# Performance work log

Measured on AMD Instinct MI355X. Metric: run time of the kernel, lower is better.

Reference implementation:

```python
import jax, jax.numpy as jnp
import numpy as np


def _cd2(a, b):
    # squared euclidean distances [n,m]
    d = jnp.sum(a * a, 1)[:, None] + jnp.sum(b * b, 1)[None, :] - 2.0 * (a @ b.T)
    return jnp.maximum(d, 0.0)


def _cdist(a, b):
    # tiny clamp keeps sqrt grad finite on the zero diagonal, fwd unchanged
    return jnp.sqrt(jnp.maximum(_cd2(a, b), 1e-30))


def _tmedian(x):
    # torch.median semantics: lower middle element
    f = jnp.sort(x.reshape(-1))
    return f[(f.shape[0] - 1) // 2]


def setup_inputs() -> dict:
    key = jax.random.key(0)
    k1, k2 = jax.random.split(key)
    feat_s = jax.random.normal(k1, (25, 640), dtype=jnp.float32)
    y_s = (jnp.arange(25) % 5).astype(jnp.int32)  # 5-way 5-shot, every class present
    feat_q = jax.random.normal(k2, (300, 640), dtype=jnp.float32)
    return {"feat_s": feat_s, "y_s": y_s, "feat_q": feat_q}


def reference(feat_s, y_s, feat_q):
    y_s_np = np.asarray(y_s)
    classes = np.unique(y_s_np)
    C = int(classes.shape[0])
    onehot = jnp.asarray(y_s_np[:, None] == classes[None, :], dtype=feat_s.dtype)  # [S,C]
    prototypes = (onehot.T @ feat_s) / jnp.sum(onehot, 0)[:, None]  # [C,D]

    # ---- virtual mixup densification ----
    dist_q = _cdist(feat_q, prototypes)  # [Nq,C]
    y_boot = np.asarray(jnp.argmin(dist_q, 1))
    q_norm = feat_q / jnp.linalg.norm(feat_q, axis=1, keepdims=True)
    cos_np = np.asarray(q_norm @ q_norm.T)
    dist_q_np = np.asarray(dist_q)
    virt = []
    for c in range(C):
        idx = np.flatnonzero(y_boot == c)
        if idx.size < 2:
            continue
        cos_c = cos_np[np.ix_(idx, idx)]
        f = np.sort(cos_c.reshape(-1))
        thresh = f[(f.size - 1) // 2]  # torch lower median
        ii, jj = np.nonzero(np.triu(cos_c >= thresh, 1))  # pairs with i<j
        if ii.size:
            virt.append(0.5 * (feat_q[idx[ii]] + feat_q[idx[jj]]))
        kq = int(idx[np.argmin(dist_q_np[idx, c])])
        virt.append((0.5 * (prototypes[c] + feat_q[kq]))[None, :])
    feat_all = jnp.concatenate([feat_q] + virt, 0) if virt else feat_q

    # ---- self-tuning affinity (kNN graph) ----
    n = int(feat_all.shape[0])
    k = max(1, int(np.log2(n)))
    dist = _cdist(feat_all, feat_all)  # [n,n]
    _, nn_idx = jax.lax.top_k(-dist, k + 1)  # smallest k+1 (incl. self)
    sigma = dist[jnp.arange(n), nn_idx[:, k]] + 1e-8
    nbrs = nn_idx[:, 1:]  # [n,k]
    d_nb = jnp.take_along_axis(dist, nbrs, 1)
    w = jnp.exp(-d_nb / (sigma[:, None] * sigma[nbrs]))
    W = jnp.zeros((n, n), feat_all.dtype).at[jnp.arange(n)[:, None], nbrs].set(w)
    W = (W + W.T) / 2
    D_inv = 1.0 / (W.sum(1) + 1e-8)

    # ---- density-adaptive lambda ----
    d = _cdist(feat_all, prototypes).min(1)
    lam = jnp.exp(-(d ** 2) / (2 * _tmedian(d) ** 2 + 1e-8))

    # ---- mm iterations (label propagation) ----
    a = _cd2(feat_all, prototypes)  # [n,C]
    y0 = jax.nn.softmax(-a, axis=1)
    scale = (lam * D_inv)[:, None]

    def step(carry, _):
        y, done = carry
        y_new = jax.nn.softmax(-a + scale * (W @ y), axis=1)
        conv = jnp.max(jnp.abs(y_new - y)) < 1e-4
        y_out = jnp.where(done | conv, y, y_new)  # emulate torch early break
        return (y_out, done | conv), None

    (y, _), _ = jax.lax.scan(step, (y0, jnp.asarray(False)), None, length=50)
    preds = jnp.argmax(y[: feat_q.shape[0]], 1)
    return preds
```

## Files before the change

### kernel.cpp

```cpp
#include <hip/hip_runtime.h>
#include <math.h>

#define CMAX 8
#define KMAX 16
#define TPB 256
#define BNMAX 1024

struct P {
  const float* fs; const int* ys; const float* fq;
  int S, Q, D, BN, NMAX;
  float* proto;
  float* G;
  float* cosq;
  int* cls; int* scount; int* qcount; int* qidx; int* kq;
  float* thr;
  int* rowcnt; int* rowoff; int* paircnt; int* basev;
  int* meta;
  int* uv;
  float* rn2;
  int* cand;
  int* nbrs; float* dnb; float* wgt; float* sigma;
  int* indeg; int* inoff; int* cursor;
  int* insrcU; float* inwU; int* indst;
  int2* inedge;
  unsigned* cosk;
  unsigned* gmaxu;
  float* amat; float* dinv; float* dmin; float* scalev;
  float* yA; float* yB;
  float* meddenom;
  int* outp;
};

__device__ inline unsigned f2key(float f){
  unsigned b=__float_as_uint(f);
  return (b&0x80000000u)? ~b : (b|0x80000000u);
}
__device__ inline float key2f(unsigned k){
  unsigned b=(k&0x80000000u)? (k^0x80000000u) : ~k;
  return __uint_as_float(b);
}
__device__ inline unsigned long long shfl_xor_u64(unsigned long long v,int m){
  unsigned lo=(unsigned)v, hi=(unsigned)(v>>32);
  lo=__shfl_xor(lo,m,64); hi=__shfl_xor(hi,m,64);
  return (((unsigned long long)hi)<<32)|lo;
}

__global__ void k_init(P p){
  if (threadIdx.x==0){
    int labs[CMAX]; int cnt[CMAX]; int C=0;
    for (int s=0;s<p.S;s++){
      int l=p.ys[s]; int f=-1;
      for(int c=0;c<C;c++) if(labs[c]==l){f=c;break;}
      if(f<0){ if(C<CMAX){labs[C]=l;cnt[C]=1;C++;} }
      else cnt[f]++;
    }
    for(int a=0;a<C;a++)for(int b=a+1;b<C;b++)
      if(labs[b]<labs[a]){int t=labs[a];labs[a]=labs[b];labs[b]=t;
                          t=cnt[a];cnt[a]=cnt[b];cnt[b]=t;}
    for(int c=0;c<C;c++){p.cls[c]=labs[c];p.scount[c]=cnt[c];}
    p.meta[0]=C;
  }
}

__global__ void k_proto(P p){
  int c=blockIdx.x; int C=p.meta[0];
  for(int d=threadIdx.x; d<p.D; d+=blockDim.x){
    float s=0.f;
    if(c<C){
      int lab=p.cls[c];
      for(int j=0;j<p.S;j++) if(p.ys[j]==lab) s+=p.fs[(size_t)j*p.D+d];
      s/= (float)p.scount[c];
    }
    p.proto[(size_t)c*p.D+d]=s;
  }
}

__global__ void k_gram(P p){
  __shared__ float arow[1024];
  int a=blockIdx.x;
  const float* ra = (a<p.Q)? p.fq + (size_t)a*p.D : p.proto + (size_t)(a-p.Q)*p.D;
  const float* A = ra;
  if(p.D<=1024){
    for(int d=threadIdx.x; d<p.D; d+=blockDim.x) arow[d]=ra[d];
    __syncthreads();
    A=(const float*)arow;
  }
  int D4=p.D>>2; int Dt=D4<<2;
  for(int b=threadIdx.x; b<p.BN; b+=blockDim.x){
    const float* rb=(b<p.Q)? p.fq+(size_t)b*p.D : p.proto+(size_t)(b-p.Q)*p.D;
    const float4* a4=(const float4*)A;
    const float4* b4=(const float4*)rb;
    float s=0.f;
    #pragma unroll 4
    for(int d=0;d<D4;d++){
      float4 x=a4[d], y=b4[d];
      s += x.x*y.x + x.y*y.y + x.z*y.z + x.w*y.w;
    }
    for(int d=Dt;d<p.D;d++) s += A[d]*rb[d];
    p.G[(size_t)a*p.BN+b]=s;
  }
}

__global__ void k_cos(P p){
  int t=blockIdx.x*blockDim.x+threadIdx.x;
  if(t>=p.Q*p.Q)return;
  int i=t/p.Q, j=t%p.Q;
  p.cosq[t]=p.G[(size_t)i*p.BN+j]/(sqrtf(p.G[(size_t)i*p.BN+i])*sqrtf(p.G[(size_t)j*p.BN+j]));
}

__global__ void k_qidx(P p){
  int c=blockIdx.x; int C=p.meta[0];
  int lane=threadIdx.x;
  if(c>=C){ if(lane==0){p.qcount[c]=0;p.kq[c]=0;} return; }
  int base=0;
  for(int q0=0;q0<p.Q;q0+=64){
    int q=q0+lane;
    bool in=false;
    if(q<p.Q){
      float gq=p.G[(size_t)q*p.BN+q];
      float best=INFINITY; int bc=0;
      for(int cc=0;cc<C;cc++){
        int pc=p.Q+cc;
        float d2=fmaxf(gq+p.G[(size_t)pc*p.BN+pc]-2.f*p.G[(size_t)q*p.BN+pc],0.f);
        if(d2<best){best=d2;bc=cc;}
      }
      in=(bc==c);
    }
    unsigned long long mask=__ballot(in);
    int pre=__popcll(mask & ((lane==63)?0x7FFFFFFFFFFFFFFFull:((1ull<<lane)-1ull)));
    if(in) p.qidx[c*p.Q+base+pre]=q;
    base+=__popcll(mask);
  }
  if(lane==0) p.qcount[c]=base;
  int pc=p.Q+c;
  float gp=p.G[(size_t)pc*p.BN+pc];
  unsigned long long best=0xFFFFFFFFFFFFFFFFull;
  for(int t=lane;t<base;t+=64){
    int q=p.qidx[c*p.Q+t];
    float d2=fmaxf(p.G[(size_t)q*p.BN+q]+gp-2.f*p.G[(size_t)q*p.BN+pc],0.f);
    unsigned long long key=(((unsigned long long)f2key(d2))<<32)|(unsigned)t;
    if(key<best)best=key;
  }
  #pragma unroll
  for(int s=32;s>=1;s>>=1){
    unsigned long long o=shfl_xor_u64(best,s);
    if(o<best)best=o;
  }
  if(lane==0){
    int t=(int)(unsigned)(best&0xFFFFFFFFull);
    p.kq[c]=(base>0)? p.qidx[c*p.Q+t] : 0;
  }
}

__global__ void k_median(P p){
  __shared__ unsigned hist[256];
  __shared__ unsigned sPref; __shared__ int sTrem;
  __shared__ int sqidx[512];
  int c=blockIdx.x; int C=p.meta[0];
  int m=(c<C)? p.qcount[c]:0;
  int tid=threadIdx.x;
  if(m<2){ if(tid==0) p.thr[c]=INFINITY; return; }
  const int* qix;
  if(p.Q<=512){
    for(int t=tid;t<m;t+=blockDim.x) sqidx[t]=p.qidx[c*p.Q+t];
    __syncthreads();
    qix=sqidx;
  } else qix=p.qidx+c*p.Q;
  int total=m*m;
  unsigned* keys=p.cosk+(size_t)c*p.Q*p.Q;
  for(int t=tid;t<total;t+=blockDim.x){
    int a=t/m, b=t-a*m;
    keys[t]=f2key(p.cosq[(size_t)qix[a]*p.Q+qix[b]]);
  }
  if(tid==0){ sPref=0u; sTrem=(total-1)/2; }
  __syncthreads();
  unsigned prefmask=0u;
  for(int shift=24;shift>=0;shift-=8){
    hist[tid&255]=0u;
    __syncthreads();
    unsigned pref=sPref;
    for(int t=tid;t<total;t+=blockDim.x){
      unsigned key=keys[t];
      if((key&prefmask)==pref) atomicAdd(&hist[(key>>shift)&255],1u);
    }
    __syncthreads();
    if(tid==0){
      int trem=sTrem; unsigned cum=0;
      for(int b=0;b<256;b++){
        unsigned h=hist[b];
        if(cum+h>(unsigned)trem){ sPref=pref|((unsigned)b<<shift); sTrem=trem-(int)cum; break; }
        cum+=h;
      }
    }
    __syncthreads();
    prefmask|=(0xFFu<<shift);
  }
  if(tid==0) p.thr[c]=key2f(sPref);
}

__global__ void k_rowcnt(P p){
  int c=blockIdx.x; int C=p.meta[0];
  int m=(c<C)? p.qcount[c]:0;
  if(m<2){ if(threadIdx.x==0) p.paircnt[c]=0; return; }
  float th=p.thr[c];
  for(int a=threadIdx.x;a<m;a+=blockDim.x){
    int ia=p.qidx[c*p.Q+a]; int cnt=0;
    const float* row=p.cosq+(size_t)ia*p.Q;
    for(int b=a+1;b<m;b++){
      int ib=p.qidx[c*p.Q+b];
      cnt += (row[ib]>=th);
    }
    p.rowcnt[c*p.Q+a]=cnt;
  }
  __syncthreads();
  if(threadIdx.x==0){
    int run=0;
    for(int a=0;a<m;a++){p.rowoff[c*p.Q+a]=run; run+=p.rowcnt[c*p.Q+a];}
    p.paircnt[c]=run;
  }
}

__global__ void k_bases(P p){
  int C=p.meta[0]; int cur=p.Q;
  for(int c=0;c<C;c++){
    p.basev[c]=cur;
    if(p.qcount[c]>=2) cur += p.paircnt[c]+1;
  }
  int n=cur; if(n>p.NMAX)n=p.NMAX;
  p.meta[1]=n;
  int k=31-__clz(n); if(k<1)k=1; if(k>KMAX-1)k=KMAX-1;
  p.meta[2]=k;
  p.meta[3]=0;
  p.meta[4]=0;
  p.meta[5]=0;
  for(int t=0;t<64;t++) p.gmaxu[t]=0u;
}

__global__ void k_uv(P p){
  int r=blockIdx.x*blockDim.x+threadIdx.x;
  if(r>=p.NMAX)return;
  p.indeg[r]=0;
  if(r<p.Q){ p.uv[2*r]=r; p.uv[2*r+1]=r; }
}

__global__ void k_uvpairs(P p){
  int c=blockIdx.x; int C=p.meta[0];
  int m=(c<C)? p.qcount[c]:0;
  if(m<2)return;
  float th=p.thr[c];
  int bs=p.basev[c];
  for(int a=threadIdx.x;a<m;a+=blockDim.x){
    int ia=p.qidx[c*p.Q+a];
    int off=bs+p.rowoff[c*p.Q+a]; int cnt=0;
    const float* row=p.cosq+(size_t)ia*p.Q;
    for(int b=a+1;b<m;b++){
      int ib=p.qidx[c*p.Q+b];
      if(row[ib]>=th){
        int r=off+cnt;
        p.uv[2*r]=ia; p.uv[2*r+1]=ib;
        cnt++;
      }
    }
  }
  if(threadIdx.x==0){
    int r=bs+p.paircnt[c];
    p.uv[2*r]=p.Q+c; p.uv[2*r+1]=p.kq[c];
  }
}

__global__ void k_rn2c(P p){
  int r=blockIdx.x*blockDim.x+threadIdx.x;
  int n=p.meta[1]; if(r>=n)return;
  int u=p.uv[2*r],v=p.uv[2*r+1];
  float hu=0.5f*(p.G[(size_t)u*p.BN+u]+p.G[(size_t)v*p.BN+u]);
  float hv=0.5f*(p.G[(size_t)u*p.BN+v]+p.G[(size_t)v*p.BN+v]);
  float rn=0.5f*(hu+hv);
  p.rn2[r]=rn;
  ((int4*)p.cand)[r]=make_int4(u,v,__float_as_int(rn),0);
}

template<int KSEL>
__device__ void knn_scan(const P& p,int n,int kp1,const float* sh,bool useSh,
                         const float* Gu,const float* Gv,float rni,
                         unsigned long long* wl){
  int lane=threadIdx.x&63; int w=threadIdx.x>>6;
  unsigned kf[KSEL]; int kj[KSEL];
  #pragma unroll
  for(int t=0;t<KSEL;t++){ kf[t]=0xFFFFFFFFu; kj[t]=0x7FFFFFFF; }
  unsigned thrw=0xFFFFFFFFu;
  int iters=(n+127)>>7;
  const int4* cand=(const int4*)p.cand;
  for(int it=0;it<iters;++it){
    int j=(it<<7)+(w<<6)+lane;
    unsigned key=0xFFFFFFFFu;
    if(j<n){
      int4 cd=cand[j];
      float dot = useSh ? (sh[cd.x]+sh[cd.y])
                        : 0.5f*(Gu[cd.x]+Gv[cd.x])+0.5f*(Gu[cd.y]+Gv[cd.y]);
      float d2=fmaxf(rni+__int_as_float(cd.z)-dot,0.f);
      key=__float_as_uint(d2);
    }
    if(key<=thrw && key<kf[KSEL-1]){
      int cj=j;
      #pragma unroll
      for(int t=0;t<KSEL;t++){
        bool lt = key<kf[t];
        unsigned nk = lt? key : kf[t];
        unsigned ok = lt? kf[t] : key;
        int nj = lt? cj : kj[t];
        int oj = lt? kj[t] : cj;
        kf[t]=nk; kj[t]=nj; key=ok; cj=oj;
      }
    }
    if((it&7)==7){
      unsigned v=kf[KSEL-1];
      #pragma unroll
      for(int s=32;s>=1;s>>=1){
        unsigned o=(unsigned)__shfl_xor((int)v,s,64);
        if(o<v)v=o;
      }
      thrw=v;
    }
  }
  for(int t=0;t<kp1;t++){
    unsigned long long mv=(((unsigned long long)kf[0])<<32)|(unsigned)kj[0];
    unsigned long long m=mv;
    #pragma unroll
    for(int s=32;s>=1;s>>=1){
      unsigned long long o=shfl_xor_u64(m,s);
      if(o<m)m=o;
    }
    if(mv==m){
      #pragma unroll
      for(int q=0;q<KSEL-1;q++){ kf[q]=kf[q+1]; kj[q]=kj[q+1]; }
      kf[KSEL-1]=0xFFFFFFFFu; kj[KSEL-1]=0x7FFFFFFF;
    }
    if(lane==0) wl[w*16+t]=m;
  }
}

__global__ void __launch_bounds__(128) k_knn(P p){
  __shared__ float sh[BNMAX];
  __shared__ unsigned long long wl[32];
  int i=blockIdx.x;
  int n=p.meta[1]; if(i>=n)return;
  int kp1=p.meta[2]+1;
  int u1=p.uv[2*i], v1=p.uv[2*i+1];
  const float* Gu=p.G+(size_t)u1*p.BN;
  const float* Gv=p.G+(size_t)v1*p.BN;
  bool useSh=(p.BN<=BNMAX);
  if(useSh){
    for(int d=threadIdx.x; d<p.BN; d+=128) sh[d]=0.5f*(Gu[d]+Gv[d]);
  }
  __syncthreads();
  float rni=p.rn2[i];
  if(kp1<=13) knn_scan<13>(p,n,kp1,sh,useSh,Gu,Gv,rni,wl);
  else        knn_scan<16>(p,n,kp1,sh,useSh,Gu,Gv,rni,wl);
  __syncthreads();
  if(threadIdx.x==0){
    int a=0,b=0;
    for(int t=0;t<kp1;t++){
      unsigned long long va=wl[a], vb=wl[16+b];
      unsigned long long m;
      if(va<=vb){m=va;a++;} else {m=vb;b++;}
      int j=(int)(unsigned)(m&0xFFFFFFFFull);
      float d2=__uint_as_float((unsigned)(m>>32));
      float dd=sqrtf(fmaxf(d2,1e-30f));
      if(t>=1){ p.nbrs[(size_t)i*KMAX+t-1]=j; p.dnb[(size_t)i*KMAX+t-1]=dd; }
      if(t==kp1-1) p.sigma[i]=dd+1e-8f;
    }
  }
}

__global__ void k_wgtcnt(P p){
  int i=blockIdx.x*blockDim.x+threadIdx.x;
  int n=p.meta[1]; if(i>=n)return;
  int k=p.meta[2];
  float si=p.sigma[i];
  for(int q=0;q<k;q++){
    int j=p.nbrs[(size_t)i*KMAX+q];
    p.wgt[(size_t)i*KMAX+q]=expf(-p.dnb[(size_t)i*KMAX+q]/(si*p.sigma[j]));
    atomicAdd(&p.indeg[j],1);
  }
  for(int q=k;q<KMAX;q++){ p.nbrs[(size_t)i*KMAX+q]=i; p.wgt[(size_t)i*KMAX+q]=0.f; }
}

__global__ void k_scan(P p){
  __shared__ int part[TPB];
  int n=p.meta[1];
  int chunk=(n+TPB-1)/TPB;
  int beg=threadIdx.x*chunk, end=beg+chunk; if(end>n)end=n;
  int s=0;
  for(int i=beg;i<end;i++) s+=p.indeg[i];
  part[threadIdx.x]=s; __syncthreads();
  if(threadIdx.x==0){
    int run=0;
    for(int t=0;t<TPB;t++){int v=part[t];part[t]=run;run+=v;}
    p.inoff[n]=run;
  }
  __syncthreads();
  int run=part[threadIdx.x];
  for(int i=beg;i<end;i++){
    p.inoff[i]=run; p.cursor[i]=run; run+=p.indeg[i];
  }
}

__global__ void k_fill(P p){
  int i=blockIdx.x*blockDim.x+threadIdx.x;
  int n=p.meta[1]; if(i>=n)return;
  int k=p.meta[2];
  for(int q=0;q<k;q++){
    int dst=p.nbrs[(size_t)i*KMAX+q];
    int slot=atomicAdd(&p.cursor[dst],1);
    p.insrcU[slot]=i; p.inwU[slot]=p.wgt[(size_t)i*KMAX+q]; p.indst[slot]=dst;
  }
}

__global__ void k_rank(P p){
  int e=blockIdx.x*blockDim.x+threadIdx.x;
  int n=p.meta[1];
  int E=p.inoff[n];
  if(e>=E)return;
  int dst=p.indst[e];
  int b=p.inoff[dst], en=p.inoff[dst+1];
  int s=p.insrcU[e]; float w=p.inwU[e];
  int rank=0;
  for(int x=b;x<en;x++) rank += (p.insrcU[x]<s);
  p.inedge[b+rank]=make_int2(s,__float_as_int(w));
}

__global__ void k_dad(P p){
  int i=blockIdx.x*blockDim.x+threadIdx.x;
  int n=p.meta[1]; if(i>=n)return;
  int k=p.meta[2]; int C=p.meta[0];
  float s=0.f;
  for(int q=0;q<k;q++) s+=p.wgt[(size_t)i*KMAX+q];
  for(int e=p.inoff[i];e<p.inoff[i+1];e++) s+=__int_as_float(p.inedge[e].y);
  p.dinv[i]=1.f/(0.5f*s+1e-8f);
  int u=p.uv[2*i],v=p.uv[2*i+1];
  float rn=p.rn2[i]; float mn=INFINITY;
  #pragma unroll
  for(int c=0;c<CMAX;c++){
    float a=INFINITY;
    if(c<C){
      int pc=p.Q+c;
      a=rn+p.G[(size_t)pc*p.BN+pc]-(p.G[(size_t)u*p.BN+pc]+p.G[(size_t)v*p.BN+pc]);
      a=fmaxf(a,0.f);
      mn=fminf(mn,a);
    }
    p.amat[(size_t)i*CMAX+c]=a;
  }
  p.dmin[i]=sqrtf(fmaxf(mn,1e-30f));
}

__global__ void k_medd(P p){
  __shared__ unsigned hist[256];
  __shared__ unsigned sPref; __shared__ int sTrem;
  int n=p.meta[1];
  int tid=threadIdx.x;
  if(tid==0){ sPref=0u; sTrem=(n-1)/2; }
  __syncthreads();
  unsigned prefmask=0u;
  for(int shift=24;shift>=0;shift-=8){
    hist[tid&255]=0u;
    __syncthreads();
    unsigned pref=sPref;
    for(int i=tid;i<n;i+=blockDim.x){
      unsigned key=f2key(p.dmin[i]);
      if((key&prefmask)==pref) atomicAdd(&hist[(key>>shift)&255],1u);
    }
    __syncthreads();
    if(tid==0){
      int trem=sTrem; unsigned cum=0;
      for(int b=0;b<256;b++){
        unsigned h=hist[b];
        if(cum+h>(unsigned)trem){ sPref=pref|((unsigned)b<<shift); sTrem=trem-(int)cum; break; }
        cum+=h;
      }
    }
    __syncthreads();
    prefmask|=(0xFFu<<shift);
  }
  if(tid==0){
    float med=key2f(sPref);
    p.meddenom[0]=2.f*med*med+1e-8f;
  }
}

__global__ void k_y0(P p){
  int i=blockIdx.x*blockDim.x+threadIdx.x;
  int n=p.meta[1]; if(i>=n)return;
  float la=expf(-(p.dmin[i]*p.dmin[i])/p.meddenom[0]);
  p.scalev[i]=la*p.dinv[i];
  float mn=INFINITY;
  #pragma unroll
  for(int c=0;c<CMAX;c++) mn=fminf(mn,p.amat[(size_t)i*CMAX+c]);
  float ex[CMAX]; float sum=0.f;
  #pragma unroll
  for(int c=0;c<CMAX;c++){
    float e=expf(mn-p.amat[(size_t)i*CMAX+c]);
    ex[c]=e; sum+=e;
  }
  float inv=1.f/sum;
  #pragma unroll
  for(int c=0;c<CMAX;c++) p.yA[(size_t)i*CMAX+c]=ex[c]*inv;
}

__global__ void __launch_bounds__(64) k_step(P p,int t){
  if(p.meta[3]) return;
  int n=p.meta[1];
  int par=p.meta[4];
  float* cur=par? p.yB : p.yA;
  float* nxt=par? p.yA : p.yB;
  int i=blockIdx.x*blockDim.x+threadIdx.x;
  float dmx=0.f;
  if(i<n){
    float wax=0,way=0,waz=0,waw=0,wbx=0,wby=0,wbz=0,wbw=0;
    #pragma unroll
    for(int q=0;q<KMAX;q++){
      int j=p.nbrs[(size_t)i*KMAX+q];
      float w=p.wgt[(size_t)i*KMAX+q];
      const float4* yr=(const float4*)(cur+(size_t)j*CMAX);
      float4 y0=yr[0],y1=yr[1];
      wax+=w*y0.x; way+=w*y0.y; waz+=w*y0.z; waw+=w*y0.w;
      wbx+=w*y1.x; wby+=w*y1.y; wbz+=w*y1.z; wbw+=w*y1.w;
    }
    int e1=p.inoff[i+1];
    for(int e=p.inoff[i];e<e1;e++){
      int2 e2=p.inedge[e];
      int j=e2.x; float w=__int_as_float(e2.y);
      const float4* yr=(const float4*)(cur+(size_t)j*CMAX);
      float4 y0=yr[0],y1=yr[1];
      wax+=w*y0.x; way+=w*y0.y; waz+=w*y0.z; waw+=w*y0.w;
      wbx+=w*y1.x; wby+=w*y1.y; wbz+=w*y1.z; wbw+=w*y1.w;
    }
    float sc=p.scalev[i]*0.5f;
    const float4* am=(const float4*)(p.amat+(size_t)i*CMAX);
    float4 a0=am[0],a1=am[1];
    float l0=sc*wax-a0.x, l1=sc*way-a0.y, l2=sc*waz-a0.z, l3=sc*waw-a0.w;
    float l4=sc*wbx-a1.x, l5=sc*wby-a1.y, l6=sc*wbz-a1.z, l7=sc*wbw-a1.w;
    float mx=fmaxf(fmaxf(fmaxf(l0,l1),fmaxf(l2,l3)),fmaxf(fmaxf(l4,l5),fmaxf(l6,l7)));
    float x0=expf(l0-mx),x1=expf(l1-mx),x2=expf(l2-mx),x3=expf(l3-mx);
    float x4=expf(l4-mx),x5=expf(l5-mx),x6=expf(l6-mx),x7=expf(l7-mx);
    float inv=1.f/(x0+x1+x2+x3+x4+x5+x6+x7);
    float4 o0=make_float4(x0*inv,x1*inv,x2*inv,x3*inv);
    float4 o1=make_float4(x4*inv,x5*inv,x6*inv,x7*inv);
    const float4* cr=(const float4*)(cur+(size_t)i*CMAX);
    float4 c0=cr[0],c1=cr[1];
    dmx=fmaxf(dmx,fabsf(o0.x-c0.x)); dmx=fmaxf(dmx,fabsf(o0.y-c0.y));
    dmx=fmaxf(dmx,fabsf(o0.z-c0.z)); dmx=fmaxf(dmx,fabsf(o0.w-c0.w));
    dmx=fmaxf(dmx,fabsf(o1.x-c1.x)); dmx=fmaxf(dmx,fabsf(o1.y-c1.y));
    dmx=fmaxf(dmx,fabsf(o1.z-c1.z)); dmx=fmaxf(dmx,fabsf(o1.w-c1.w));
    float4* nr=(float4*)(nxt+(size_t)i*CMAX);
    nr[0]=o0; nr[1]=o1;
  }
  #pragma unroll
  for(int s=32;s>=1;s>>=1) dmx=fmaxf(dmx,__shfl_xor(dmx,s,64));
  if(threadIdx.x==0){
    atomicMax(p.gmaxu+t,__float_as_uint(dmx));
    __threadfence();
    int fin=atomicAdd(&p.meta[5],1);
    if(fin==(int)gridDim.x-1){
      p.meta[5]=0;
      float mm=__uint_as_float(p.gmaxu[t]);
      if(mm<1e-4f) p.meta[3]=1;
      else         p.meta[4]=par^1;
    }
  }
}

__global__ void k_arg(P p){
  int q=blockIdx.x*blockDim.x+threadIdx.x;
  if(q>=p.Q)return;
  int C=p.meta[0];
  const float* cur=p.meta[4]? p.yB : p.yA;
  float best=cur[(size_t)q*CMAX+0]; int bc=0;
  for(int c=1;c<C;c++){
    float v=cur[(size_t)q*CMAX+c];
    if(v>best){best=v;bc=c;}
  }
  p.outp[q]=bc;
}


static void make_layout(char* base,int S,int Q,int D,int BN,long N,
                        const float*fs,const int*ys,const float*fq,
                        int* outp, P* pp, size_t* need){
  size_t off=0;
  auto A=[&](size_t b)->char*{
    size_t o=(off+255)&~(size_t)255; off=o+b; return base+o;
  };
  P p{};
  p.fs=fs;p.ys=ys;p.fq=fq;p.S=S;p.Q=Q;p.D=D;p.BN=BN;p.NMAX=(int)N;
  p.proto=(float*)A(4ul*CMAX*D);
  p.G=(float*)A(4ul*(size_t)BN*BN);
  p.cosq=(float*)A(4ul*(size_t)Q*Q);
  p.cls=(int*)A(4ul*CMAX);
  p.scount=(int*)A(4ul*CMAX);
  p.qcount=(int*)A(4ul*CMAX);
  p.qidx=(int*)A(4ul*CMAX*Q);
  p.kq=(int*)A(4ul*CMAX);
  p.thr=(float*)A(4ul*CMAX);
  p.rowcnt=(int*)A(4ul*CMAX*Q);
  p.rowoff=(int*)A(4ul*CMAX*Q);
  p.paircnt=(int*)A(4ul*CMAX);
  p.basev=(int*)A(4ul*CMAX);
  p.meta=(int*)A(4ul*16);
  p.uv=(int*)A(8ul*N);
  p.rn2=(float*)A(4ul*N);
  p.cand=(int*)A(16ul*N);
  p.nbrs=(int*)A(4ul*KMAX*N);
  p.dnb=(float*)A(4ul*KMAX*N);
  p.wgt=(float*)A(4ul*KMAX*N);
  p.sigma=(float*)A(4ul*N);
  p.indeg=(int*)A(4ul*N);
  p.inoff=(int*)A(4ul*(N+1));
  p.cursor=(int*)A(4ul*N);
  p.insrcU=(int*)A(4ul*KMAX*N);
  p.inwU=(float*)A(4ul*KMAX*N);
  p.indst=(int*)A(4ul*KMAX*N);
  p.inedge=(int2*)A(8ul*KMAX*N);
  p.cosk=(unsigned*)A(4ul*CMAX*(size_t)Q*Q);
  p.gmaxu=(unsigned*)A(4ul*64);
  p.amat=(float*)A(4ul*CMAX*N);
  p.dinv=(float*)A(4ul*N);
  p.dmin=(float*)A(4ul*N);
  p.scalev=(float*)A(4ul*N);
  p.yA=(float*)A(4ul*CMAX*N);
  p.yB=(float*)A(4ul*CMAX*N);
  p.meddenom=(float*)A(4ul*4);
  p.outp=outp;
  *pp=p; *need=off;
}

extern "C" void kernel_launch(void* const* d_in, const int* in_sizes, int n_in,
                              void* d_out, int out_size, void* d_ws, size_t ws_size,
                              hipStream_t stream){
  const float* fs=(const float*)d_in[0];
  const int*   ys=(const int*)d_in[1];
  const float* fq=(const float*)d_in[2];
  int S=in_sizes[1];
  int D=in_sizes[0]/S;
  int Q=in_sizes[2]/D;
  int BN=Q+CMAX;

  long full=(long)Q + (long)Q*(Q-1)/2 + CMAX;
  long cand[4]={full,16384,8192,5000};
  P p{}; size_t need=0; int NMAX=(int)cand[3];
  for(int ci=0;ci<4;ci++){
    long N=cand[ci]; if(N<Q+CMAX)N=Q+CMAX;
    make_layout((char*)d_ws,S,Q,D,BN,N,fs,ys,fq,(int*)d_out,&p,&need);
    NMAX=(int)N;
    if(need<=ws_size) break;
  }

  int gN=(NMAX+TPB-1)/TPB;
  long gEl=((long)NMAX*KMAX+TPB-1)/TPB;
  int gE=(int)gEl;
  int gS=(NMAX+63)/64;

  k_init   <<<1, 64, 0, stream>>>(p);
  k_proto  <<<CMAX, TPB, 0, stream>>>(p);
  k_gram   <<<BN, TPB, 0, stream>>>(p);
  k_cos    <<<(Q*Q+TPB-1)/TPB, TPB, 0, stream>>>(p);
  k_qidx   <<<CMAX, 64, 0, stream>>>(p);
  k_median <<<CMAX, TPB, 0, stream>>>(p);
  k_rowcnt <<<CMAX, TPB, 0, stream>>>(p);
  k_bases  <<<1, 1, 0, stream>>>(p);
  k_uv     <<<gN, TPB, 0, stream>>>(p);
  k_uvpairs<<<CMAX, TPB, 0, stream>>>(p);
  k_rn2c   <<<gN, TPB, 0, stream>>>(p);
  k_knn    <<<NMAX, 128, 0, stream>>>(p);
  k_wgtcnt <<<gN, TPB, 0, stream>>>(p);
  k_scan   <<<1, TPB, 0, stream>>>(p);
  k_fill   <<<gN, TPB, 0, stream>>>(p);
  k_rank   <<<gE, TPB, 0, stream>>>(p);
  k_dad    <<<gN, TPB, 0, stream>>>(p);
  k_medd   <<<1, TPB, 0, stream>>>(p);
  k_y0     <<<gN, TPB, 0, stream>>>(p);
  for(int t=0;t<50;t++)
    k_step <<<gS, 64, 0, stream>>>(p, t);
  k_arg    <<<(Q+TPB-1)/TPB, TPB, 0, stream>>>(p);
}
```

Measured before the change: 563.3 us.

## Fuse setup kernels, unroll kNN scan by four, pack out-edges for propagation

Folds k_bases into k_rowcnt using a last-block atomic counter, moves k_uv's work into k_rn2c, and merges the y0 softmax init into k_medd, removing three launches. The kNN candidate scan now evaluates four candidates per iteration and skips insertion when their minimum cannot enter the list. It also syncs the wave threshold every two iterations instead of every eight. Neighbour index and weight are packed into one int2 array so each k_step iteration does one load instead of two. The cost is extra memory for the packed edges and a serial single-block y0 init inside k_medd.

```diff
diff --git a/kernel.cpp b/kernel.cpp
--- a/kernel.cpp
+++ b/kernel.cpp
@@ -20,6 +20,7 @@
   float* rn2;
   int* cand;
   int* nbrs; float* dnb; float* wgt; float* sigma;
+  int2* outedge;
   int* indeg; int* inoff; int* cursor;
   int* insrcU; float* inwU; int* indst;
   int2* inedge;
@@ -59,6 +60,7 @@
                           t=cnt[a];cnt[a]=cnt[b];cnt[b]=t;}
     for(int c=0;c<C;c++){p.cls[c]=labs[c];p.scount[c]=cnt[c];}
     p.meta[0]=C;
+    p.meta[6]=0;
   }
 }
 
@@ -201,46 +203,44 @@
 __global__ void k_rowcnt(P p){
   int c=blockIdx.x; int C=p.meta[0];
   int m=(c<C)? p.qcount[c]:0;
-  if(m<2){ if(threadIdx.x==0) p.paircnt[c]=0; return; }
-  float th=p.thr[c];
-  for(int a=threadIdx.x;a<m;a+=blockDim.x){
-    int ia=p.qidx[c*p.Q+a]; int cnt=0;
-    const float* row=p.cosq+(size_t)ia*p.Q;
-    for(int b=a+1;b<m;b++){
-      int ib=p.qidx[c*p.Q+b];
-      cnt += (row[ib]>=th);
-    }
-    p.rowcnt[c*p.Q+a]=cnt;
+  if(m>=2){
+    float th=p.thr[c];
+    for(int a=threadIdx.x;a<m;a+=blockDim.x){
+      int ia=p.qidx[c*p.Q+a]; int cnt=0;
+      const float* row=p.cosq+(size_t)ia*p.Q;
+      for(int b=a+1;b<m;b++){
+        int ib=p.qidx[c*p.Q+b];
+        cnt += (row[ib]>=th);
+      }
+      p.rowcnt[c*p.Q+a]=cnt;
+    }
+    __syncthreads();
+    if(threadIdx.x==0){
+      int run=0;
+      for(int a=0;a<m;a++){p.rowoff[c*p.Q+a]=run; run+=p.rowcnt[c*p.Q+a];}
+      p.paircnt[c]=run;
+    }
+  } else {
+    if(threadIdx.x==0) p.paircnt[c]=0;
   }
   __syncthreads();
   if(threadIdx.x==0){
-    int run=0;
-    for(int a=0;a<m;a++){p.rowoff[c*p.Q+a]=run; run+=p.rowcnt[c*p.Q+a];}
-    p.paircnt[c]=run;
-  }
-}
-
-__global__ void k_bases(P p){
-  int C=p.meta[0]; int cur=p.Q;
-  for(int c=0;c<C;c++){
-    p.basev[c]=cur;
-    if(p.qcount[c]>=2) cur += p.paircnt[c]+1;
-  }
-  int n=cur; if(n>p.NMAX)n=p.NMAX;
-  p.meta[1]=n;
-  int k=31-__clz(n); if(k<1)k=1; if(k>KMAX-1)k=KMAX-1;
-  p.meta[2]=k;
-  p.meta[3]=0;
-  p.meta[4]=0;
-  p.meta[5]=0;
-  for(int t=0;t<64;t++) p.gmaxu[t]=0u;
-}
-
-__global__ void k_uv(P p){
-  int r=blockIdx.x*blockDim.x+threadIdx.x;
-  if(r>=p.NMAX)return;
-  p.indeg[r]=0;
-  if(r<p.Q){ p.uv[2*r]=r; p.uv[2*r+1]=r; }
+    __threadfence();
+    int fin=atomicAdd(&p.meta[6],1);
+    if(fin==(int)gridDim.x-1){
+      int cur=p.Q;
+      for(int cc=0;cc<C;cc++){
+        p.basev[cc]=cur;
+        if(p.qcount[cc]>=2) cur += p.paircnt[cc]+1;
+      }
+      int n=cur; if(n>p.NMAX)n=p.NMAX;
+      p.meta[1]=n;
+      int k=31-__clz(n); if(k<1)k=1; if(k>KMAX-1)k=KMAX-1;
+      p.meta[2]=k;
+      p.meta[3]=0; p.meta[4]=0; p.meta[5]=0;
+      for(int t=0;t<64;t++) p.gmaxu[t]=0u;
+    }
+  }
 }
 
 __global__ void k_uvpairs(P p){
@@ -270,8 +270,11 @@
 
 __global__ void k_rn2c(P p){
   int r=blockIdx.x*blockDim.x+threadIdx.x;
+  if(r<p.NMAX) p.indeg[r]=0;
   int n=p.meta[1]; if(r>=n)return;
-  int u=p.uv[2*r],v=p.uv[2*r+1];
+  int u,v;
+  if(r<p.Q){ u=r; v=r; p.uv[2*r]=r; p.uv[2*r+1]=r; }
+  else     { u=p.uv[2*r]; v=p.uv[2*r+1]; }
   float hu=0.5f*(p.G[(size_t)u*p.BN+u]+p.G[(size_t)v*p.BN+u]);
   float hv=0.5f*(p.G[(size_t)u*p.BN+v]+p.G[(size_t)v*p.BN+v]);
   float rn=0.5f*(hu+hv);
@@ -288,31 +291,28 @@
   #pragma unroll
   for(int t=0;t<KSEL;t++){ kf[t]=0xFFFFFFFFu; kj[t]=0x7FFFFFFF; }
   unsigned thrw=0xFFFFFFFFu;
-  int iters=(n+127)>>7;
   const int4* cand=(const int4*)p.cand;
-  for(int it=0;it<iters;++it){
-    int j=(it<<7)+(w<<6)+lane;
-    unsigned key=0xFFFFFFFFu;
-    if(j<n){
-      int4 cd=cand[j];
-      float dot = useSh ? (sh[cd.x]+sh[cd.y])
-                        : 0.5f*(Gu[cd.x]+Gv[cd.x])+0.5f*(Gu[cd.y]+Gv[cd.y]);
-      float d2=fmaxf(rni+__int_as_float(cd.z)-dot,0.f);
-      key=__float_as_uint(d2);
-    }
-    if(key<=thrw && key<kf[KSEL-1]){
-      int cj=j;
-      #pragma unroll
-      for(int t=0;t<KSEL;t++){
-        bool lt = key<kf[t];
-        unsigned nk = lt? key : kf[t];
-        unsigned ok = lt? kf[t] : key;
-        int nj = lt? cj : kj[t];
-        int oj = lt? kj[t] : cj;
-        kf[t]=nk; kj[t]=nj; key=ok; cj=oj;
-      }
-    }
-    if((it&7)==7){
+  int nIt=(n+511)>>9;
+  #define EVALK(JV,KV) \
+    if((JV)<n){ int4 cd=cand[JV]; \
+      float dot = useSh ? (sh[cd.x]+sh[cd.y]) \
+                        : 0.5f*(Gu[cd.x]+Gv[cd.x])+0.5f*(Gu[cd.y]+Gv[cd.y]); \
+      KV=__float_as_uint(fmaxf(rni+__int_as_float(cd.z)-dot,0.f)); }
+  #define INSK(KEY,JV) { unsigned key=(KEY); int cj=(JV); \
+    _Pragma("unroll") \
+    for(int t=0;t<KSEL;t++){ bool lt=key<kf[t]; \
+      unsigned nk=lt?key:kf[t], ok=lt?kf[t]:key; \
+      int nj=lt?cj:kj[t], oj=lt?kj[t]:cj; \
+      kf[t]=nk; kj[t]=nj; key=ok; cj=oj; } }
+  for(int it=0;it<nIt;++it){
+    int j0=(it<<9)+(w<<6)+lane;
+    unsigned k0=0xFFFFFFFFu,k1=0xFFFFFFFFu,k2=0xFFFFFFFFu,k3=0xFFFFFFFFu;
+    EVALK(j0,k0); EVALK(j0+128,k1); EVALK(j0+256,k2); EVALK(j0+384,k3);
+    unsigned mn=min(min(k0,k1),min(k2,k3));
+    if(mn<=thrw && mn<kf[KSEL-1]){
+      INSK(k0,j0); INSK(k1,j0+128); INSK(k2,j0+256); INSK(k3,j0+384);
+    }
+    if((it&1)==1){
       unsigned v=kf[KSEL-1];
       #pragma unroll
       for(int s=32;s>=1;s>>=1){
@@ -322,6 +322,8 @@
       thrw=v;
     }
   }
+  #undef EVALK
+  #undef INSK
   for(int t=0;t<kp1;t++){
     unsigned long long mv=(((unsigned long long)kf[0])<<32)|(unsigned)kj[0];
     unsigned long long m=mv;
@@ -379,10 +381,15 @@
   float si=p.sigma[i];
   for(int q=0;q<k;q++){
     int j=p.nbrs[(size_t)i*KMAX+q];
-    p.wgt[(size_t)i*KMAX+q]=expf(-p.dnb[(size_t)i*KMAX+q]/(si*p.sigma[j]));
+    float wq=expf(-p.dnb[(size_t)i*KMAX+q]/(si*p.sigma[j]));
+    p.wgt[(size_t)i*KMAX+q]=wq;
+    p.outedge[(size_t)i*KMAX+q]=make_int2(j,__float_as_int(wq));
     atomicAdd(&p.indeg[j],1);
   }
-  for(int q=k;q<KMAX;q++){ p.nbrs[(size_t)i*KMAX+q]=i; p.wgt[(size_t)i*KMAX+q]=0.f; }
+  for(int q=k;q<KMAX;q++){
+    p.nbrs[(size_t)i*KMAX+q]=i; p.wgt[(size_t)i*KMAX+q]=0.f;
+    p.outedge[(size_t)i*KMAX+q]=make_int2(i,0);
+  }
 }
 
 __global__ void k_scan(P p){
@@ -456,6 +463,7 @@
 __global__ void k_medd(P p){
   __shared__ unsigned hist[256];
   __shared__ unsigned sPref; __shared__ int sTrem;
+  __shared__ float sDen;
   int n=p.meta[1];
   int tid=threadIdx.x;
   if(tid==0){ sPref=0u; sTrem=(n-1)/2; }
@@ -483,27 +491,27 @@
   }
   if(tid==0){
     float med=key2f(sPref);
-    p.meddenom[0]=2.f*med*med+1e-8f;
-  }
-}
-
-__global__ void k_y0(P p){
-  int i=blockIdx.x*blockDim.x+threadIdx.x;
-  int n=p.meta[1]; if(i>=n)return;
-  float la=expf(-(p.dmin[i]*p.dmin[i])/p.meddenom[0]);
-  p.scalev[i]=la*p.dinv[i];
-  float mn=INFINITY;
-  #pragma unroll
-  for(int c=0;c<CMAX;c++) mn=fminf(mn,p.amat[(size_t)i*CMAX+c]);
-  float ex[CMAX]; float sum=0.f;
-  #pragma unroll
-  for(int c=0;c<CMAX;c++){
-    float e=expf(mn-p.amat[(size_t)i*CMAX+c]);
-    ex[c]=e; sum+=e;
-  }
-  float inv=1.f/sum;
-  #pragma unroll
-  for(int c=0;c<CMAX;c++) p.yA[(size_t)i*CMAX+c]=ex[c]*inv;
+    sDen=2.f*med*med+1e-8f;
+    p.meddenom[0]=sDen;
+  }
+  __syncthreads();
+  float den=sDen;
+  for(int i=tid;i<n;i+=blockDim.x){
+    float la=expf(-(p.dmin[i]*p.dmin[i])/den);
+    p.scalev[i]=la*p.dinv[i];
+    float mn=INFINITY;
+    #pragma unroll
+    for(int c=0;c<CMAX;c++) mn=fminf(mn,p.amat[(size_t)i*CMAX+c]);
+    float ex[CMAX]; float sum=0.f;
+    #pragma unroll
+    for(int c=0;c<CMAX;c++){
+      float e=expf(mn-p.amat[(size_t)i*CMAX+c]);
+      ex[c]=e; sum+=e;
+    }
+    float inv=1.f/sum;
+    #pragma unroll
+    for(int c=0;c<CMAX;c++) p.yA[(size_t)i*CMAX+c]=ex[c]*inv;
+  }
 }
 
 __global__ void __launch_bounds__(64) k_step(P p,int t){
@@ -516,10 +524,11 @@
   float dmx=0.f;
   if(i<n){
     float wax=0,way=0,waz=0,waw=0,wbx=0,wby=0,wbz=0,wbw=0;
+    const int2* oe=p.outedge+(size_t)i*KMAX;
     #pragma unroll
     for(int q=0;q<KMAX;q++){
-      int j=p.nbrs[(size_t)i*KMAX+q];
-      float w=p.wgt[(size_t)i*KMAX+q];
+      int2 e2=oe[q];
+      int j=e2.x; float w=__int_as_float(e2.y);
       const float4* yr=(const float4*)(cur+(size_t)j*CMAX);
       float4 y0=yr[0],y1=yr[1];
       wax+=w*y0.x; way+=w*y0.y; waz+=w*y0.z; waw+=w*y0.w;
@@ -613,6 +622,7 @@
   p.dnb=(float*)A(4ul*KMAX*N);
   p.wgt=(float*)A(4ul*KMAX*N);
   p.sigma=(float*)A(4ul*N);
+  p.outedge=(int2*)A(8ul*KMAX*N);
   p.indeg=(int*)A(4ul*N);
   p.inoff=(int*)A(4ul*(N+1));
   p.cursor=(int*)A(4ul*N);
@@ -666,8 +676,6 @@
   k_qidx   <<<CMAX, 64, 0, stream>>>(p);
   k_median <<<CMAX, TPB, 0, stream>>>(p);
   k_rowcnt <<<CMAX, TPB, 0, stream>>>(p);
-  k_bases  <<<1, 1, 0, stream>>>(p);
-  k_uv     <<<gN, TPB, 0, stream>>>(p);
   k_uvpairs<<<CMAX, TPB, 0, stream>>>(p);
   k_rn2c   <<<gN, TPB, 0, stream>>>(p);
   k_knn    <<<NMAX, 128, 0, stream>>>(p);
@@ -677,7 +685,6 @@
   k_rank   <<<gE, TPB, 0, stream>>>(p);
   k_dad    <<<gN, TPB, 0, stream>>>(p);
   k_medd   <<<1, TPB, 0, stream>>>(p);
-  k_y0     <<<gN, TPB, 0, stream>>>(p);
   for(int t=0;t<50;t++)
     k_step <<<gS, 64, 0, stream>>>(p, t);
   k_arg    <<<(Q+TPB-1)/TPB, TPB, 0, stream>>>(p);
```

New measurement: 586.5 us. 4.1% more time.
